# Performance work log

Measured on AMD Instinct MI355X. Metric: run time of the kernel, lower is better.

## Reference

```python
import jax, jax.numpy as jnp
import numpy as np

E, D, H, K = 8, 768, 3072, 2   # num_experts, embed_size, expert_size, top-k
TAU = 1.0
BN, PN = 32, 196

def l2norm(v):
    # F.normalize(p=2, dim=-1), eps=1e-12
    return v / jnp.maximum(jnp.linalg.norm(v, axis=-1, keepdims=True), 1e-12)

def setup_inputs() -> dict:
    key = jax.random.key(0)
    ks = jax.random.split(key, 8)
    s = 0.02  # weight init scale for stability
    return {
        "x": jax.random.normal(ks[0], (BN, PN, D), dtype=jnp.float32),
        "Wlinear": jax.random.normal(ks[1], (D, D), dtype=jnp.float32) * s,
        "learnedE": jax.random.normal(ks[2], (E, D), dtype=jnp.float32),
        "bias": jnp.zeros((BN * PN, E), dtype=jnp.float32),
        "W1": jax.random.normal(ks[3], (E, D, H), dtype=jnp.float32) * s,
        "b1": jnp.zeros((E, H), dtype=jnp.float32),
        "W2": jax.random.normal(ks[4], (E, H, D), dtype=jnp.float32) * s,
        "b2": jnp.zeros((E, D), dtype=jnp.float32),
        "sW1": jax.random.normal(ks[5], (D, H), dtype=jnp.float32) * s,
        "sb1": jnp.zeros((H,), dtype=jnp.float32),
        "sW2": jax.random.normal(ks[6], (H, D), dtype=jnp.float32) * s,
        "sb2": jnp.zeros((D,), dtype=jnp.float32),
    }

def reference(x, Wlinear, learnedE, bias, W1, b1, W2, b2, sW1, sb1, sW2, sb2):
    bn, pn, d = x.shape
    patches = x.reshape(bn * pn, d)                      # [T, D]
    proj = l2norm(patches @ Wlinear.T)                   # router projection
    routed = proj @ l2norm(learnedE).T                   # [T, E] cosine scores
    probs = jax.nn.softmax((routed + bias) / TAU, axis=1)  # eval path (no noise)
    k_probs, k_idx = jax.lax.top_k(probs, K)             # [T, K]
    # combine weights: scatter top-k probs into dense [T, E] gate matrix
    T = probs.shape[0]
    gates = jnp.zeros_like(probs).at[jnp.arange(T)[:, None], k_idx].add(k_probs)
    # expert MLPs computed densely for all experts, masked by gates
    h = jax.nn.gelu(jnp.einsum('td,edh->teh', patches, W1) + b1[None], approximate=False)
    eo = jnp.einsum('teh,ehd->ted', h, W2) + b2[None]    # [T, E, D]
    moe = jnp.einsum('ted,te->td', eo, gates)            # weighted combine
    # shared expert (expert_list[-1]) applied to every token; dropout is identity in eval
    shared = jax.nn.gelu(patches @ sW1 + sb1, approximate=False) @ sW2 + sb2
    return (moe + shared).reshape(bn, pn, d)
```

## Files before the change

### kernel.cpp

```cpp
#include <hip/hip_runtime.h>
#include <hip/hip_bf16.h>

typedef __hip_bfloat16 bf16;
typedef __attribute__((ext_vector_type(8))) short short8;
typedef __attribute__((ext_vector_type(4))) float f32x4;

#define T_TOK 6272
#define D_DIM 768
#define H_DIM 3072
#define NEXP 8
#define MAXTILES 160
#define BKR 64

#define S_BARRIER() __builtin_amdgcn_s_barrier()
#define WAIT_VM4() asm volatile("s_waitcnt vmcnt(4)" ::: "memory")
#define WAIT_VM0() asm volatile("s_waitcnt vmcnt(0)" ::: "memory")
#define WAIT_LGKM0() asm volatile("s_waitcnt lgkmcnt(0)" ::: "memory")

__device__ __forceinline__ void async16(void* lds, const void* g) {
  __builtin_amdgcn_global_load_lds(
      (const __attribute__((address_space(1))) void*)g,
      (__attribute__((address_space(3))) void*)lds, 16, 0, 0);
}

__device__ __forceinline__ float gelu_f(float x) {
  float z = x * 0.70710678118654752f;
  float az = fabsf(z);
  float t = 1.f / (1.f + 0.3275911f * az);
  float poly = ((((1.061405429f * t - 1.453152027f) * t + 1.421413741f) * t -
                 0.284496736f) * t + 0.254829592f) * t;
  float e = __expf(-az * az);
  float er = 1.f - poly * e;
  er = copysignf(er, z);
  return 0.5f * x * (1.f + er);
}


__global__ void cast_hilo(const float* __restrict__ in, bf16* __restrict__ hi,
                          bf16* __restrict__ lo, int n) {
  int i = blockIdx.x * blockDim.x + threadIdx.x;
  int stride = gridDim.x * blockDim.x;
  for (; i < n; i += stride) {
    float x = in[i];
    bf16 h = __float2bfloat16(x);
    hi[i] = h;
    lo[i] = __float2bfloat16(x - __bfloat162float(h));
  }
}

__global__ void transpose_cast(const float* __restrict__ in, bf16* __restrict__ out,
                               int R, int C) {
  __shared__ float tile[32][33];
  int b = blockIdx.z;
  const float* ib = in + (size_t)b * R * C;
  bf16* ob = out + (size_t)b * R * C;
  int r0 = blockIdx.x * 32, c0 = blockIdx.y * 32;
  int tx = threadIdx.x & 31, ty = threadIdx.x >> 5;
  for (int i = 0; i < 32; i += 8)
    tile[ty + i][tx] = ib[(size_t)(r0 + ty + i) * C + c0 + tx];
  __syncthreads();
  for (int i = 0; i < 32; i += 8)
    ob[(size_t)(c0 + ty + i) * R + r0 + tx] = __float2bfloat16(tile[tx][ty + i]);
}

__global__ void norm_learnedE(const float* __restrict__ lE, float* __restrict__ eHat) {
  int wave = threadIdx.x >> 6, lane = threadIdx.x & 63;
  for (int e = wave; e < NEXP; e += 4) {
    float v[12];
    float ss = 0.f;
    for (int j = 0; j < 12; j++) {
      v[j] = lE[e * D_DIM + lane + 64 * j];
      ss += v[j] * v[j];
    }
    for (int o = 32; o; o >>= 1) ss += __shfl_xor(ss, o);
    float rn = 1.f / fmaxf(sqrtf(ss), 1e-12f);
    for (int j = 0; j < 12; j++) eHat[e * D_DIM + lane + 64 * j] = v[j] * rn;
  }
}


__global__ __launch_bounds__(256, 2) void gemm_router(
    const bf16* __restrict__ pHi, const bf16* __restrict__ pLo,
    const bf16* __restrict__ wHi, const bf16* __restrict__ wLo,
    float* __restrict__ y) {
  __shared__ __align__(16) bf16 As[2][128 * BKR];
  __shared__ __align__(16) bf16 Bs[2][128 * BKR];
  int tid = threadIdx.x, wave = tid >> 6, lane = tid & 63;
  int wr = wave >> 1, wc = wave & 1;
  int rowbase = blockIdx.x * 128, colbase = blockIdx.y * 128;
  int rslot = (lane & 7) ^ (lane >> 3);

  size_t aoff[4], boff[4];
#pragma unroll
  for (int c = 0; c < 4; c++) {
    int row = 32 * wave + 8 * c + (lane >> 3);
    aoff[c] = (size_t)(rowbase + row) * D_DIM + rslot * 8;
    boff[c] = (size_t)(colbase + row) * D_DIM + rslot * 8;
  }

  auto stage = [&](int buf, int ks) {
    int term = ks / 12;
    const bf16* A = (term == 1) ? pLo : pHi;
    const bf16* B = (term == 2) ? wLo : wHi;
    int kk = (ks - term * 12) * BKR;
#pragma unroll
    for (int c = 0; c < 4; c++) {
      async16(&As[buf][(32 * wave + 8 * c) * BKR], A + aoff[c] + kk);
      async16(&Bs[buf][(32 * wave + 8 * c) * BKR], B + boff[c] + kk);
    }
  };

  f32x4 acc[4][4];
#pragma unroll
  for (int m = 0; m < 4; m++)
#pragma unroll
    for (int n = 0; n < 4; n++) acc[m][n] = 0.f;

  stage(0, 0);
  __syncthreads();
  int cur = 0;
  int q = lane >> 4, fr = lane & 15;
  for (int ks = 0; ks < 36; ks++) {
    if (ks < 35) stage(cur ^ 1, ks + 1);
    const bf16* Ac = As[cur];
    const bf16* Bc = Bs[cur];
#pragma unroll
    for (int kh = 0; kh < 2; kh++) {
      short8 af[4], bfr[4];
#pragma unroll
      for (int m = 0; m < 4; m++) {
        int row = wr * 64 + m * 16 + fr;
        int ls = ((kh << 2) + q) ^ (row & 7);
        af[m] = *(const short8*)&Ac[row * BKR + ls * 8];
      }
#pragma unroll
      for (int n = 0; n < 4; n++) {
        int row = wc * 64 + n * 16 + fr;
        int ls = ((kh << 2) + q) ^ (row & 7);
        bfr[n] = *(const short8*)&Bc[row * BKR + ls * 8];
      }
#pragma unroll
      for (int m = 0; m < 4; m++)
#pragma unroll
        for (int n = 0; n < 4; n++)
          acc[m][n] = __builtin_amdgcn_mfma_f32_16x16x32_bf16(af[m], bfr[n], acc[m][n], 0, 0, 0);
    }
    __syncthreads();
    cur ^= 1;
  }
  for (int m = 0; m < 4; m++)
    for (int n = 0; n < 4; n++)
      for (int j = 0; j < 4; j++) {
        int r = rowbase + wr * 64 + m * 16 + (lane >> 4) * 4 + j;
        int c = colbase + wc * 64 + n * 16 + (lane & 15);
        y[(size_t)r * D_DIM + c] = acc[m][n][j];
      }
}


__global__ void router_epi(const float* __restrict__ y, const float* __restrict__ eHat,
                           const float* __restrict__ bias, int* __restrict__ gidx,
                           float* __restrict__ gval, int* __restrict__ counts) {
  int wave = threadIdx.x >> 6, lane = threadIdx.x & 63;
  int t = blockIdx.x * 4 + wave;
  float v[12];
  float ss = 0.f;
  for (int j = 0; j < 12; j++) {
    v[j] = y[(size_t)t * D_DIM + lane + 64 * j];
    ss += v[j] * v[j];
  }
  for (int o = 32; o; o >>= 1) ss += __shfl_xor(ss, o);
  float d[NEXP];
  for (int e = 0; e < NEXP; e++) {
    float s = 0.f;
    for (int j = 0; j < 12; j++) s += v[j] * eHat[e * D_DIM + lane + 64 * j];
    for (int o = 32; o; o >>= 1) s += __shfl_xor(s, o);
    d[e] = s;
  }
  if (lane == 0) {
    float rn = 1.f / fmaxf(sqrtf(ss), 1e-12f);
    float sc[NEXP], mx = -1e30f;
    for (int e = 0; e < NEXP; e++) {
      sc[e] = d[e] * rn + bias[t * NEXP + e];
      mx = fmaxf(mx, sc[e]);
    }
    float p[NEXP], sum = 0.f;
    for (int e = 0; e < NEXP; e++) {
      p[e] = expf(sc[e] - mx);
      sum += p[e];
    }
    float inv = 1.f / sum;
    int i1 = 0;
    for (int e = 1; e < NEXP; e++)
      if (sc[e] > sc[i1]) i1 = e;
    int i2 = -1;
    for (int e = 0; e < NEXP; e++) {
      if (e == i1) continue;
      if (i2 < 0 || sc[e] > sc[i2]) i2 = e;
    }
    gidx[t * 2] = i1;
    gidx[t * 2 + 1] = i2;
    gval[t * 2] = p[i1] * inv;
    gval[t * 2 + 1] = p[i2] * inv;
    atomicAdd(&counts[i1], 1);
    atomicAdd(&counts[i2], 1);
  }
}


__global__ void scan_build(const int* __restrict__ counts, int* __restrict__ segstart,
                           int* __restrict__ cursors, int* __restrict__ tiles,
                           int* __restrict__ numtiles) {
  if (threadIdx.x == 0) {
    int off = 0;
    for (int e = 0; e < NEXP; e++) {
      segstart[e] = off;
      cursors[e] = off;
      off += counts[e];
    }
    segstart[NEXP] = off;
    segstart[NEXP + 1] = off + T_TOK;
    int nt = 0;
    for (int e = 0; e < NEXP + 1; e++) {
      int cnt = (e < NEXP) ? counts[e] : T_TOK;
      int ntl = (cnt + 127) >> 7;
      for (int l = 0; l < ntl; l++) {
        tiles[nt * 2] = e;
        tiles[nt * 2 + 1] = l;
        nt++;
      }
    }
    *numtiles = nt;
  }
}

__global__ void fill_assign(const int* __restrict__ gidx, int* __restrict__ cursors,
                            int* __restrict__ rowtok, int* __restrict__ slot_of) {
  int t = blockIdx.x * 256 + threadIdx.x;
  if (t >= T_TOK) return;
  for (int k = 0; k < 2; k++) {
    int e = gidx[t * 2 + k];
    int pos = atomicAdd(&cursors[e], 1);
    rowtok[pos] = t;
    slot_of[t * 2 + k] = pos;
  }
  rowtok[2 * T_TOK + t] = t;
}



__global__ __launch_bounds__(256, 4) void gemm_ffn1(
    const bf16* __restrict__ pHi, const bf16* __restrict__ W1T,
    const bf16* __restrict__ sW1T, const float* __restrict__ b1,
    const float* __restrict__ sb1, const int* __restrict__ segstart,
    const int* __restrict__ tiles, const int* __restrict__ numtiles,
    const int* __restrict__ rowtok, bf16* __restrict__ hbuf) {
  int gx = blockIdx.x;
  if (gx >= *numtiles) return;
  int seg = tiles[gx * 2], lt = tiles[gx * 2 + 1];
  int s0 = segstart[seg] + lt * 128;
  int send = segstart[seg + 1];
  const bf16* Bw = (seg < NEXP) ? W1T + (size_t)seg * H_DIM * D_DIM : sW1T;
  const float* bb = (seg < NEXP) ? b1 + seg * H_DIM : sb1;

  __shared__ __align__(16) bf16 As[2][128 * 32];
  __shared__ __align__(16) bf16 Bs[2][128 * 32];
  int tid = threadIdx.x, wave = tid >> 6, lane = tid & 63;
  int wr = wave >> 1, wc = wave & 1;
  int colbase = blockIdx.y * 128;
  int g8 = (((lane & 3) ^ ((lane >> 3) & 3))) * 8;

  const bf16* aptr[2];
  const bf16* bptr[2];
#pragma unroll
  for (int p = 0; p < 2; p++) {
    int r = wave * 32 + p * 16 + (lane >> 2);
    int s = s0 + r;
    if (s > send - 1) s = send - 1;
    aptr[p] = pHi + (size_t)rowtok[s] * D_DIM + g8;
    bptr[p] = Bw + (size_t)(colbase + r) * D_DIM + g8;
  }

  auto stage = [&](int buf, int ks) {
    int kk = ks * 32;
#pragma unroll
    for (int p = 0; p < 2; p++) {
      async16(&As[buf][(wave * 32 + p * 16) * 32], aptr[p] + kk);
      async16(&Bs[buf][(wave * 32 + p * 16) * 32], bptr[p] + kk);
    }
  };

  f32x4 acc[4][4];
#pragma unroll
  for (int m = 0; m < 4; m++)
#pragma unroll
    for (int n = 0; n < 4; n++) acc[m][n] = 0.f;

  WAIT_VM0();
  stage(0, 0);
  stage(1, 1);

  int q = lane >> 4, fr = lane & 15;
  int ls8 = (q ^ ((fr >> 1) & 3)) * 8;

#define NT1 24
  for (int ks = 0; ks < NT1; ks++) {
    if (ks + 1 < NT1) { WAIT_VM4(); } else { WAIT_VM0(); }
    S_BARRIER();
    const bf16* Ac = As[ks & 1];
    const bf16* Bc = Bs[ks & 1];
    short8 af[4], bfr[4];
#pragma unroll
    for (int m = 0; m < 4; m++)
      af[m] = *(const short8*)&Ac[(wr * 64 + m * 16 + fr) * 32 + ls8];
#pragma unroll
    for (int n = 0; n < 4; n++)
      bfr[n] = *(const short8*)&Bc[(wc * 64 + n * 16 + fr) * 32 + ls8];
    __builtin_amdgcn_s_setprio(1);
#pragma unroll
    for (int m = 0; m < 4; m++)
#pragma unroll
      for (int n = 0; n < 4; n++)
        acc[m][n] = __builtin_amdgcn_mfma_f32_16x16x32_bf16(af[m], bfr[n], acc[m][n], 0, 0, 0);
    __builtin_amdgcn_s_setprio(0);
    WAIT_LGKM0();
    S_BARRIER();
    if (ks + 2 < NT1) stage(ks & 1, ks + 2);
  }
#pragma unroll
  for (int n = 0; n < 4; n++) {
    int c = colbase + wc * 64 + n * 16 + (lane & 15);
    float bv = bb[c];
#pragma unroll
    for (int m = 0; m < 4; m++)
#pragma unroll
      for (int j = 0; j < 4; j++) {
        int s = s0 + wr * 64 + m * 16 + (lane >> 4) * 4 + j;
        if (s < send) {
          float xv = acc[m][n][j] + bv;
          hbuf[(size_t)s * H_DIM + c] = __float2bfloat16(gelu_f(xv));
        }
      }
  }
}


__global__ __launch_bounds__(256, 4) void gemm_ffn2(
    const bf16* __restrict__ hbuf, const bf16* __restrict__ W2T,
    const bf16* __restrict__ sW2T, const float* __restrict__ b2,
    const float* __restrict__ sb2, const int* __restrict__ segstart,
    const int* __restrict__ tiles, const int* __restrict__ numtiles,
    float* __restrict__ moebuf) {
  int gx = blockIdx.x;
  if (gx >= *numtiles) return;
  int seg = tiles[gx * 2], lt = tiles[gx * 2 + 1];
  int s0 = segstart[seg] + lt * 128;
  int send = segstart[seg + 1];
  const bf16* Bw = (seg < NEXP) ? W2T + (size_t)seg * H_DIM * D_DIM : sW2T;
  const float* bb = (seg < NEXP) ? b2 + seg * D_DIM : sb2;

  __shared__ __align__(16) bf16 As[2][128 * 32];
  __shared__ __align__(16) bf16 Bs[2][128 * 32];
  int tid = threadIdx.x, wave = tid >> 6, lane = tid & 63;
  int wr = wave >> 1, wc = wave & 1;
  int colbase = blockIdx.y * 128;
  int g8 = (((lane & 3) ^ ((lane >> 3) & 3))) * 8;

  const bf16* aptr[2];
  const bf16* bptr[2];
#pragma unroll
  for (int p = 0; p < 2; p++) {
    int r = wave * 32 + p * 16 + (lane >> 2);
    int s = s0 + r;
    if (s > send - 1) s = send - 1;
    aptr[p] = hbuf + (size_t)s * H_DIM + g8;
    bptr[p] = Bw + (size_t)(colbase + r) * H_DIM + g8;
  }

  auto stage = [&](int buf, int ks) {
    int kk = ks * 32;
#pragma unroll
    for (int p = 0; p < 2; p++) {
      async16(&As[buf][(wave * 32 + p * 16) * 32], aptr[p] + kk);
      async16(&Bs[buf][(wave * 32 + p * 16) * 32], bptr[p] + kk);
    }
  };

  f32x4 acc[4][4];
#pragma unroll
  for (int m = 0; m < 4; m++)
#pragma unroll
    for (int n = 0; n < 4; n++) acc[m][n] = 0.f;

  WAIT_VM0();
  stage(0, 0);
  stage(1, 1);

  int q = lane >> 4, fr = lane & 15;
  int ls8 = (q ^ ((fr >> 1) & 3)) * 8;

#define NT2 96
  for (int ks = 0; ks < NT2; ks++) {
    if (ks + 1 < NT2) { WAIT_VM4(); } else { WAIT_VM0(); }
    S_BARRIER();
    const bf16* Ac = As[ks & 1];
    const bf16* Bc = Bs[ks & 1];
    short8 af[4], bfr[4];
#pragma unroll
    for (int m = 0; m < 4; m++)
      af[m] = *(const short8*)&Ac[(wr * 64 + m * 16 + fr) * 32 + ls8];
#pragma unroll
    for (int n = 0; n < 4; n++)
      bfr[n] = *(const short8*)&Bc[(wc * 64 + n * 16 + fr) * 32 + ls8];
    __builtin_amdgcn_s_setprio(1);
#pragma unroll
    for (int m = 0; m < 4; m++)
#pragma unroll
      for (int n = 0; n < 4; n++)
        acc[m][n] = __builtin_amdgcn_mfma_f32_16x16x32_bf16(af[m], bfr[n], acc[m][n], 0, 0, 0);
    __builtin_amdgcn_s_setprio(0);
    WAIT_LGKM0();
    S_BARRIER();
    if (ks + 2 < NT2) stage(ks & 1, ks + 2);
  }
#pragma unroll
  for (int n = 0; n < 4; n++) {
    int c = colbase + wc * 64 + n * 16 + (lane & 15);
    float bv = bb[c];
#pragma unroll
    for (int m = 0; m < 4; m++)
#pragma unroll
      for (int j = 0; j < 4; j++) {
        int s = s0 + wr * 64 + m * 16 + (lane >> 4) * 4 + j;
        if (s < send) moebuf[(size_t)s * D_DIM + c] = acc[m][n][j] + bv;
      }
  }
}


__global__ void combine_out(const float* __restrict__ moebuf, const float* __restrict__ gval,
                            const int* __restrict__ slot_of, float* __restrict__ out) {
  int i = blockIdx.x * 256 + threadIdx.x;
  const int total = T_TOK * (D_DIM / 4);
  if (i >= total) return;
  int t = i / (D_DIM / 4), c = i % (D_DIM / 4);
  float g0 = gval[2 * t], g1 = gval[2 * t + 1];
  int sA = slot_of[2 * t], sB = slot_of[2 * t + 1];
  const f32x4* pa = (const f32x4*)(moebuf + (size_t)sA * D_DIM) + c;
  const f32x4* pb = (const f32x4*)(moebuf + (size_t)sB * D_DIM) + c;
  const f32x4* ps = (const f32x4*)(moebuf + (size_t)(2 * T_TOK + t) * D_DIM) + c;
  f32x4 r = g0 * (*pa) + g1 * (*pb) + *ps;
  ((f32x4*)out)[i] = r;
}


extern "C" void kernel_launch(void* const* d_in, const int* in_sizes, int n_in,
                              void* d_out, int out_size, void* d_ws, size_t ws_size,
                              hipStream_t stream) {
  const float* x = (const float*)d_in[0];
  const float* Wlinear = (const float*)d_in[1];
  const float* learnedE = (const float*)d_in[2];
  const float* bias = (const float*)d_in[3];
  const float* W1 = (const float*)d_in[4];
  const float* b1 = (const float*)d_in[5];
  const float* W2 = (const float*)d_in[6];
  const float* b2 = (const float*)d_in[7];
  const float* sW1 = (const float*)d_in[8];
  const float* sb1 = (const float*)d_in[9];
  const float* sW2 = (const float*)d_in[10];
  const float* sb2 = (const float*)d_in[11];
  float* out = (float*)d_out;

  char* ws = (char*)d_ws;
  size_t off = 0;
  auto alloc = [&](size_t bytes) {
    char* p = ws + off;
    off += (bytes + 255) & ~(size_t)255;
    return p;
  };
  float* eHat = (float*)alloc(8 * 768 * 4);
  bf16* pHi = (bf16*)alloc((size_t)T_TOK * D_DIM * 2);
  bf16* pLo = (bf16*)alloc((size_t)T_TOK * D_DIM * 2);
  bf16* wHi = (bf16*)alloc((size_t)D_DIM * D_DIM * 2);
  bf16* wLo = (bf16*)alloc((size_t)D_DIM * D_DIM * 2);
  bf16* W1T = (bf16*)alloc((size_t)NEXP * D_DIM * H_DIM * 2);
  bf16* W2T = (bf16*)alloc((size_t)NEXP * D_DIM * H_DIM * 2);
  bf16* sW1T = (bf16*)alloc((size_t)D_DIM * H_DIM * 2);
  bf16* sW2T = (bf16*)alloc((size_t)D_DIM * H_DIM * 2);
  float* y = (float*)alloc((size_t)T_TOK * D_DIM * 4);
  bf16* hbuf = (bf16*)alloc((size_t)3 * T_TOK * H_DIM * 2);
  float* moebuf = (float*)alloc((size_t)3 * T_TOK * D_DIM * 4);
  int* gidx = (int*)alloc(T_TOK * 2 * 4);
  float* gval = (float*)alloc(T_TOK * 2 * 4);
  int* rowtok = (int*)alloc(3 * T_TOK * 4);
  int* slot_of = (int*)alloc(T_TOK * 2 * 4);
  int* counts = (int*)alloc(8 * 4);
  int* segstart = (int*)alloc(10 * 4);
  int* cursors = (int*)alloc(8 * 4);
  int* numtiles = (int*)alloc(4);
  int* tiles = (int*)alloc(MAXTILES * 2 * 4);
  (void)ws_size; (void)in_sizes; (void)n_in; (void)out_size;

  hipMemsetAsync(counts, 0, 8 * 4, stream);
  norm_learnedE<<<1, 256, 0, stream>>>(learnedE, eHat);
  cast_hilo<<<2048, 256, 0, stream>>>(x, pHi, pLo, T_TOK * D_DIM);
  cast_hilo<<<1024, 256, 0, stream>>>(Wlinear, wHi, wLo, D_DIM * D_DIM);
  transpose_cast<<<dim3(D_DIM / 32, H_DIM / 32, NEXP), 256, 0, stream>>>(W1, W1T, D_DIM, H_DIM);
  transpose_cast<<<dim3(H_DIM / 32, D_DIM / 32, NEXP), 256, 0, stream>>>(W2, W2T, H_DIM, D_DIM);
  transpose_cast<<<dim3(D_DIM / 32, H_DIM / 32, 1), 256, 0, stream>>>(sW1, sW1T, D_DIM, H_DIM);
  transpose_cast<<<dim3(H_DIM / 32, D_DIM / 32, 1), 256, 0, stream>>>(sW2, sW2T, H_DIM, D_DIM);

  gemm_router<<<dim3(T_TOK / 128, D_DIM / 128), 256, 0, stream>>>(pHi, pLo, wHi, wLo, y);
  router_epi<<<T_TOK / 4, 256, 0, stream>>>(y, eHat, bias, gidx, gval, counts);
  scan_build<<<1, 64, 0, stream>>>(counts, segstart, cursors, tiles, numtiles);
  fill_assign<<<(T_TOK + 255) / 256, 256, 0, stream>>>(gidx, cursors, rowtok, slot_of);

  gemm_ffn1<<<dim3(MAXTILES, H_DIM / 128), 256, 0, stream>>>(
      pHi, W1T, sW1T, b1, sb1, segstart, tiles, numtiles, rowtok, hbuf);
  gemm_ffn2<<<dim3(MAXTILES, D_DIM / 128), 256, 0, stream>>>(
      hbuf, W2T, sW2T, b2, sb2, segstart, tiles, numtiles, moebuf);

  combine_out<<<(T_TOK * (D_DIM / 4) + 255) / 256, 256, 0, stream>>>(moebuf, gval, slot_of, out);
}
```

Baseline: 723.1 us.

## Enlarge expert FFN GEMM tiles to 256x256x64 with 512-thread blocks

```diff
diff --git a/kernel.cpp b/kernel.cpp
--- a/kernel.cpp
+++ b/kernel.cpp
@@ -9,11 +9,11 @@
 #define D_DIM 768
 #define H_DIM 3072
 #define NEXP 8
-#define MAXTILES 160
+#define MAXT 96
 #define BKR 64
 
 #define S_BARRIER() __builtin_amdgcn_s_barrier()
-#define WAIT_VM4() asm volatile("s_waitcnt vmcnt(4)" ::: "memory")
+#define WAIT_VM8() asm volatile("s_waitcnt vmcnt(8)" ::: "memory")
 #define WAIT_VM0() asm volatile("s_waitcnt vmcnt(0)" ::: "memory")
 #define WAIT_LGKM0() asm volatile("s_waitcnt lgkmcnt(0)" ::: "memory")
 
@@ -223,7 +223,7 @@
     int nt = 0;
     for (int e = 0; e < NEXP + 1; e++) {
       int cnt = (e < NEXP) ? counts[e] : T_TOK;
-      int ntl = (cnt + 127) >> 7;
+      int ntl = (cnt + 255) >> 8;
       for (int l = 0; l < ntl; l++) {
         tiles[nt * 2] = e;
         tiles[nt * 2 + 1] = l;
@@ -249,7 +249,7 @@
 
 
 
-__global__ __launch_bounds__(256, 4) void gemm_ffn1(
+__global__ __launch_bounds__(512, 2) void gemm_ffn1(
     const bf16* __restrict__ pHi, const bf16* __restrict__ W1T,
     const bf16* __restrict__ sW1T, const float* __restrict__ b1,
     const float* __restrict__ sb1, const int* __restrict__ segstart,
@@ -258,41 +258,41 @@
   int gx = blockIdx.x;
   if (gx >= *numtiles) return;
   int seg = tiles[gx * 2], lt = tiles[gx * 2 + 1];
-  int s0 = segstart[seg] + lt * 128;
+  int s0 = segstart[seg] + lt * 256;
   int send = segstart[seg + 1];
   const bf16* Bw = (seg < NEXP) ? W1T + (size_t)seg * H_DIM * D_DIM : sW1T;
   const float* bb = (seg < NEXP) ? b1 + seg * H_DIM : sb1;
 
-  __shared__ __align__(16) bf16 As[2][128 * 32];
-  __shared__ __align__(16) bf16 Bs[2][128 * 32];
+  __shared__ __align__(16) bf16 As[2][256 * 64];
+  __shared__ __align__(16) bf16 Bs[2][256 * 64];
   int tid = threadIdx.x, wave = tid >> 6, lane = tid & 63;
-  int wr = wave >> 1, wc = wave & 1;
-  int colbase = blockIdx.y * 128;
-  int g8 = (((lane & 3) ^ ((lane >> 3) & 3))) * 8;
-
-  const bf16* aptr[2];
-  const bf16* bptr[2];
-#pragma unroll
-  for (int p = 0; p < 2; p++) {
-    int r = wave * 32 + p * 16 + (lane >> 2);
+  int wr = wave >> 2, wc = wave & 3;
+  int colbase = blockIdx.y * 256;
+  int g8 = ((lane & 7) ^ (lane >> 3)) * 8;
+
+  const bf16* aptr[4];
+  const bf16* bptr[4];
+#pragma unroll
+  for (int j = 0; j < 4; j++) {
+    int r = wave * 32 + j * 8 + (lane >> 3);
     int s = s0 + r;
     if (s > send - 1) s = send - 1;
-    aptr[p] = pHi + (size_t)rowtok[s] * D_DIM + g8;
-    bptr[p] = Bw + (size_t)(colbase + r) * D_DIM + g8;
-  }
-
-  auto stage = [&](int buf, int ks) {
-    int kk = ks * 32;
-#pragma unroll
-    for (int p = 0; p < 2; p++) {
-      async16(&As[buf][(wave * 32 + p * 16) * 32], aptr[p] + kk);
-      async16(&Bs[buf][(wave * 32 + p * 16) * 32], bptr[p] + kk);
+    aptr[j] = pHi + (size_t)rowtok[s] * D_DIM + g8;
+    bptr[j] = Bw + (size_t)(colbase + r) * D_DIM + g8;
+  }
+
+  auto stage = [&](int buf, int kt) {
+    int kk = kt * 64;
+#pragma unroll
+    for (int j = 0; j < 4; j++) {
+      async16(&As[buf][(wave * 32 + j * 8) * 64], aptr[j] + kk);
+      async16(&Bs[buf][(wave * 32 + j * 8) * 64], bptr[j] + kk);
     }
   };
 
-  f32x4 acc[4][4];
-#pragma unroll
-  for (int m = 0; m < 4; m++)
+  f32x4 acc[8][4];
+#pragma unroll
+  for (int m = 0; m < 8; m++)
 #pragma unroll
     for (int n = 0; n < 4; n++) acc[m][n] = 0.f;
 
@@ -301,41 +301,44 @@
   stage(1, 1);
 
   int q = lane >> 4, fr = lane & 15;
-  int ls8 = (q ^ ((fr >> 1) & 3)) * 8;
-
-#define NT1 24
-  for (int ks = 0; ks < NT1; ks++) {
-    if (ks + 1 < NT1) { WAIT_VM4(); } else { WAIT_VM0(); }
+  int frs = fr & 7;
+
+#define NT1 12
+  for (int kt = 0; kt < NT1; kt++) {
+    if (kt + 1 < NT1) { WAIT_VM8(); } else { WAIT_VM0(); }
     S_BARRIER();
-    const bf16* Ac = As[ks & 1];
-    const bf16* Bc = Bs[ks & 1];
-    short8 af[4], bfr[4];
-#pragma unroll
-    for (int m = 0; m < 4; m++)
-      af[m] = *(const short8*)&Ac[(wr * 64 + m * 16 + fr) * 32 + ls8];
-#pragma unroll
-    for (int n = 0; n < 4; n++)
-      bfr[n] = *(const short8*)&Bc[(wc * 64 + n * 16 + fr) * 32 + ls8];
-    __builtin_amdgcn_s_setprio(1);
-#pragma unroll
-    for (int m = 0; m < 4; m++)
-#pragma unroll
-      for (int n = 0; n < 4; n++)
-        acc[m][n] = __builtin_amdgcn_mfma_f32_16x16x32_bf16(af[m], bfr[n], acc[m][n], 0, 0, 0);
-    __builtin_amdgcn_s_setprio(0);
+    const bf16* Ac = As[kt & 1];
+    const bf16* Bc = Bs[kt & 1];
+#pragma unroll
+    for (int kh = 0; kh < 2; kh++) {
+      int ls8 = (((kh << 2) + q) ^ frs) * 8;
+      short8 af[8];
+#pragma unroll
+      for (int m = 0; m < 8; m++)
+        af[m] = *(const short8*)&Ac[(wr * 128 + m * 16 + fr) * 64 + ls8];
+      __builtin_amdgcn_s_setprio(1);
+#pragma unroll
+      for (int n = 0; n < 4; n++) {
+        short8 bfr = *(const short8*)&Bc[(wc * 64 + n * 16 + fr) * 64 + ls8];
+#pragma unroll
+        for (int m = 0; m < 8; m++)
+          acc[m][n] = __builtin_amdgcn_mfma_f32_16x16x32_bf16(af[m], bfr, acc[m][n], 0, 0, 0);
+      }
+      __builtin_amdgcn_s_setprio(0);
+    }
     WAIT_LGKM0();
     S_BARRIER();
-    if (ks + 2 < NT1) stage(ks & 1, ks + 2);
+    if (kt + 2 < NT1) stage(kt & 1, kt + 2);
   }
 #pragma unroll
   for (int n = 0; n < 4; n++) {
-    int c = colbase + wc * 64 + n * 16 + (lane & 15);
+    int c = colbase + wc * 64 + n * 16 + fr;
     float bv = bb[c];
 #pragma unroll
-    for (int m = 0; m < 4; m++)
+    for (int m = 0; m < 8; m++)
 #pragma unroll
       for (int j = 0; j < 4; j++) {
-        int s = s0 + wr * 64 + m * 16 + (lane >> 4) * 4 + j;
+        int s = s0 + wr * 128 + m * 16 + q * 4 + j;
         if (s < send) {
           float xv = acc[m][n][j] + bv;
           hbuf[(size_t)s * H_DIM + c] = __float2bfloat16(gelu_f(xv));
@@ -345,7 +348,7 @@
 }
 
 
-__global__ __launch_bounds__(256, 4) void gemm_ffn2(
+__global__ __launch_bounds__(512, 2) void gemm_ffn2(
     const bf16* __restrict__ hbuf, const bf16* __restrict__ W2T,
     const bf16* __restrict__ sW2T, const float* __restrict__ b2,
     const float* __restrict__ sb2, const int* __restrict__ segstart,
@@ -354,41 +357,41 @@
   int gx = blockIdx.x;
   if (gx >= *numtiles) return;
   int seg = tiles[gx * 2], lt = tiles[gx * 2 + 1];
-  int s0 = segstart[seg] + lt * 128;
+  int s0 = segstart[seg] + lt * 256;
   int send = segstart[seg + 1];
   const bf16* Bw = (seg < NEXP) ? W2T + (size_t)seg * H_DIM * D_DIM : sW2T;
   const float* bb = (seg < NEXP) ? b2 + seg * D_DIM : sb2;
 
-  __shared__ __align__(16) bf16 As[2][128 * 32];
-  __shared__ __align__(16) bf16 Bs[2][128 * 32];
+  __shared__ __align__(16) bf16 As[2][256 * 64];
+  __shared__ __align__(16) bf16 Bs[2][256 * 64];
   int tid = threadIdx.x, wave = tid >> 6, lane = tid & 63;
-  int wr = wave >> 1, wc = wave & 1;
-  int colbase = blockIdx.y * 128;
-  int g8 = (((lane & 3) ^ ((lane >> 3) & 3))) * 8;
-
-  const bf16* aptr[2];
-  const bf16* bptr[2];
-#pragma unroll
-  for (int p = 0; p < 2; p++) {
-    int r = wave * 32 + p * 16 + (lane >> 2);
+  int wr = wave >> 2, wc = wave & 3;
+  int colbase = blockIdx.y * 256;
+  int g8 = ((lane & 7) ^ (lane >> 3)) * 8;
+
+  const bf16* aptr[4];
+  const bf16* bptr[4];
+#pragma unroll
+  for (int j = 0; j < 4; j++) {
+    int r = wave * 32 + j * 8 + (lane >> 3);
     int s = s0 + r;
     if (s > send - 1) s = send - 1;
-    aptr[p] = hbuf + (size_t)s * H_DIM + g8;
-    bptr[p] = Bw + (size_t)(colbase + r) * H_DIM + g8;
-  }
-
-  auto stage = [&](int buf, int ks) {
-    int kk = ks * 32;
-#pragma unroll
-    for (int p = 0; p < 2; p++) {
-      async16(&As[buf][(wave * 32 + p * 16) * 32], aptr[p] + kk);
-      async16(&Bs[buf][(wave * 32 + p * 16) * 32], bptr[p] + kk);
+    aptr[j] = hbuf + (size_t)s * H_DIM + g8;
+    bptr[j] = Bw + (size_t)(colbase + r) * H_DIM + g8;
+  }
+
+  auto stage = [&](int buf, int kt) {
+    int kk = kt * 64;
+#pragma unroll
+    for (int j = 0; j < 4; j++) {
+      async16(&As[buf][(wave * 32 + j * 8) * 64], aptr[j] + kk);
+      async16(&Bs[buf][(wave * 32 + j * 8) * 64], bptr[j] + kk);
     }
   };
 
-  f32x4 acc[4][4];
-#pragma unroll
-  for (int m = 0; m < 4; m++)
+  f32x4 acc[8][4];
+#pragma unroll
+  for (int m = 0; m < 8; m++)
 #pragma unroll
     for (int n = 0; n < 4; n++) acc[m][n] = 0.f;
 
@@ -397,41 +400,44 @@
   stage(1, 1);
 
   int q = lane >> 4, fr = lane & 15;
-  int ls8 = (q ^ ((fr >> 1) & 3)) * 8;
-
-#define NT2 96
-  for (int ks = 0; ks < NT2; ks++) {
-    if (ks + 1 < NT2) { WAIT_VM4(); } else { WAIT_VM0(); }
+  int frs = fr & 7;
+
+#define NT2 48
+  for (int kt = 0; kt < NT2; kt++) {
+    if (kt + 1 < NT2) { WAIT_VM8(); } else { WAIT_VM0(); }
     S_BARRIER();
-    const bf16* Ac = As[ks & 1];
-    const bf16* Bc = Bs[ks & 1];
-    short8 af[4], bfr[4];
-#pragma unroll
-    for (int m = 0; m < 4; m++)
-      af[m] = *(const short8*)&Ac[(wr * 64 + m * 16 + fr) * 32 + ls8];
-#pragma unroll
-    for (int n = 0; n < 4; n++)
-      bfr[n] = *(const short8*)&Bc[(wc * 64 + n * 16 + fr) * 32 + ls8];
-    __builtin_amdgcn_s_setprio(1);
-#pragma unroll
-    for (int m = 0; m < 4; m++)
-#pragma unroll
-      for (int n = 0; n < 4; n++)
-        acc[m][n] = __builtin_amdgcn_mfma_f32_16x16x32_bf16(af[m], bfr[n], acc[m][n], 0, 0, 0);
-    __builtin_amdgcn_s_setprio(0);
+    const bf16* Ac = As[kt & 1];
+    const bf16* Bc = Bs[kt & 1];
+#pragma unroll
+    for (int kh = 0; kh < 2; kh++) {
+      int ls8 = (((kh << 2) + q) ^ frs) * 8;
+      short8 af[8];
+#pragma unroll
+      for (int m = 0; m < 8; m++)
+        af[m] = *(const short8*)&Ac[(wr * 128 + m * 16 + fr) * 64 + ls8];
+      __builtin_amdgcn_s_setprio(1);
+#pragma unroll
+      for (int n = 0; n < 4; n++) {
+        short8 bfr = *(const short8*)&Bc[(wc * 64 + n * 16 + fr) * 64 + ls8];
+#pragma unroll
+        for (int m = 0; m < 8; m++)
+          acc[m][n] = __builtin_amdgcn_mfma_f32_16x16x32_bf16(af[m], bfr, acc[m][n], 0, 0, 0);
+      }
+      __builtin_amdgcn_s_setprio(0);
+    }
     WAIT_LGKM0();
     S_BARRIER();
-    if (ks + 2 < NT2) stage(ks & 1, ks + 2);
+    if (kt + 2 < NT2) stage(kt & 1, kt + 2);
   }
 #pragma unroll
   for (int n = 0; n < 4; n++) {
-    int c = colbase + wc * 64 + n * 16 + (lane & 15);
+    int c = colbase + wc * 64 + n * 16 + fr;
     float bv = bb[c];
 #pragma unroll
-    for (int m = 0; m < 4; m++)
+    for (int m = 0; m < 8; m++)
 #pragma unroll
       for (int j = 0; j < 4; j++) {
-        int s = s0 + wr * 64 + m * 16 + (lane >> 4) * 4 + j;
+        int s = s0 + wr * 128 + m * 16 + q * 4 + j;
         if (s < send) moebuf[(size_t)s * D_DIM + c] = acc[m][n][j] + bv;
       }
   }
@@ -498,7 +504,7 @@
   int* segstart = (int*)alloc(10 * 4);
   int* cursors = (int*)alloc(8 * 4);
   int* numtiles = (int*)alloc(4);
-  int* tiles = (int*)alloc(MAXTILES * 2 * 4);
+  int* tiles = (int*)alloc(MAXT * 2 * 4);
   (void)ws_size; (void)in_sizes; (void)n_in; (void)out_size;
 
   hipMemsetAsync(counts, 0, 8 * 4, stream);
@@ -515,9 +521,9 @@
   scan_build<<<1, 64, 0, stream>>>(counts, segstart, cursors, tiles, numtiles);
   fill_assign<<<(T_TOK + 255) / 256, 256, 0, stream>>>(gidx, cursors, rowtok, slot_of);
 
-  gemm_ffn1<<<dim3(MAXTILES, H_DIM / 128), 256, 0, stream>>>(
+  gemm_ffn1<<<dim3(MAXT, H_DIM / 256), 512, 0, stream>>>(
       pHi, W1T, sW1T, b1, sb1, segstart, tiles, numtiles, rowtok, hbuf);
-  gemm_ffn2<<<dim3(MAXTILES, D_DIM / 128), 256, 0, stream>>>(
+  gemm_ffn2<<<dim3(MAXT, D_DIM / 256), 512, 0, stream>>>(
       hbuf, W2T, sW2T, b2, sb2, segstart, tiles, numtiles, moebuf);
 
   combine_out<<<(T_TOK * (D_DIM / 4) + 255) / 256, 256, 0, stream>>>(moebuf, gval, slot_of, out);
```

After: 825.2 us. +14.1%, slower.

## Load A fragments directly from global to registers, stage only B in LDS

Applied to the files above, without the earlier changes.

```diff
diff --git a/kernel.cpp b/kernel.cpp
--- a/kernel.cpp
+++ b/kernel.cpp
@@ -13,7 +13,7 @@
 #define BKR 64
 
 #define S_BARRIER() __builtin_amdgcn_s_barrier()
-#define WAIT_VM4() asm volatile("s_waitcnt vmcnt(4)" ::: "memory")
+#define WAIT_VM2() asm volatile("s_waitcnt vmcnt(2)" ::: "memory")
 #define WAIT_VM0() asm volatile("s_waitcnt vmcnt(0)" ::: "memory")
 #define WAIT_LGKM0() asm volatile("s_waitcnt lgkmcnt(0)" ::: "memory")
 
@@ -263,31 +263,33 @@
   const bf16* Bw = (seg < NEXP) ? W1T + (size_t)seg * H_DIM * D_DIM : sW1T;
   const float* bb = (seg < NEXP) ? b1 + seg * H_DIM : sb1;
 
-  __shared__ __align__(16) bf16 As[2][128 * 32];
   __shared__ __align__(16) bf16 Bs[2][128 * 32];
   int tid = threadIdx.x, wave = tid >> 6, lane = tid & 63;
   int wr = wave >> 1, wc = wave & 1;
   int colbase = blockIdx.y * 128;
+  int q = lane >> 4, fr = lane & 15;
   int g8 = (((lane & 3) ^ ((lane >> 3) & 3))) * 8;
-
-  const bf16* aptr[2];
+  int ls8 = (q ^ ((fr >> 1) & 3)) * 8;
+
   const bf16* bptr[2];
 #pragma unroll
   for (int p = 0; p < 2; p++) {
     int r = wave * 32 + p * 16 + (lane >> 2);
-    int s = s0 + r;
+    bptr[p] = Bw + (size_t)(colbase + r) * D_DIM + g8;
+  }
+  const bf16* arow[4];
+#pragma unroll
+  for (int m = 0; m < 4; m++) {
+    int s = s0 + wr * 64 + m * 16 + fr;
     if (s > send - 1) s = send - 1;
-    aptr[p] = pHi + (size_t)rowtok[s] * D_DIM + g8;
-    bptr[p] = Bw + (size_t)(colbase + r) * D_DIM + g8;
-  }
-
-  auto stage = [&](int buf, int ks) {
+    arow[m] = pHi + (size_t)rowtok[s] * D_DIM + q * 8;
+  }
+
+  auto stageB = [&](int buf, int ks) {
     int kk = ks * 32;
 #pragma unroll
-    for (int p = 0; p < 2; p++) {
-      async16(&As[buf][(wave * 32 + p * 16) * 32], aptr[p] + kk);
+    for (int p = 0; p < 2; p++)
       async16(&Bs[buf][(wave * 32 + p * 16) * 32], bptr[p] + kk);
-    }
   };
 
   f32x4 acc[4][4];
@@ -297,22 +299,18 @@
     for (int n = 0; n < 4; n++) acc[m][n] = 0.f;
 
   WAIT_VM0();
-  stage(0, 0);
-  stage(1, 1);
-
-  int q = lane >> 4, fr = lane & 15;
-  int ls8 = (q ^ ((fr >> 1) & 3)) * 8;
+  short8 af[4];
+#pragma unroll
+  for (int m = 0; m < 4; m++) af[m] = *(const short8*)arow[m];
+  stageB(0, 0);
+  stageB(1, 1);
 
 #define NT1 24
   for (int ks = 0; ks < NT1; ks++) {
-    if (ks + 1 < NT1) { WAIT_VM4(); } else { WAIT_VM0(); }
+    if (ks + 1 < NT1) { WAIT_VM2(); } else { WAIT_VM0(); }
     S_BARRIER();
-    const bf16* Ac = As[ks & 1];
     const bf16* Bc = Bs[ks & 1];
-    short8 af[4], bfr[4];
-#pragma unroll
-    for (int m = 0; m < 4; m++)
-      af[m] = *(const short8*)&Ac[(wr * 64 + m * 16 + fr) * 32 + ls8];
+    short8 bfr[4];
 #pragma unroll
     for (int n = 0; n < 4; n++)
       bfr[n] = *(const short8*)&Bc[(wc * 64 + n * 16 + fr) * 32 + ls8];
@@ -325,17 +323,22 @@
     __builtin_amdgcn_s_setprio(0);
     WAIT_LGKM0();
     S_BARRIER();
-    if (ks + 2 < NT1) stage(ks & 1, ks + 2);
+    if (ks + 1 < NT1) {
+      int kk = (ks + 1) * 32;
+#pragma unroll
+      for (int m = 0; m < 4; m++) af[m] = *(const short8*)(arow[m] + kk);
+      if (ks + 2 < NT1) stageB(ks & 1, ks + 2);
+    }
   }
 #pragma unroll
   for (int n = 0; n < 4; n++) {
-    int c = colbase + wc * 64 + n * 16 + (lane & 15);
+    int c = colbase + wc * 64 + n * 16 + fr;
     float bv = bb[c];
 #pragma unroll
     for (int m = 0; m < 4; m++)
 #pragma unroll
       for (int j = 0; j < 4; j++) {
-        int s = s0 + wr * 64 + m * 16 + (lane >> 4) * 4 + j;
+        int s = s0 + wr * 64 + m * 16 + q * 4 + j;
         if (s < send) {
           float xv = acc[m][n][j] + bv;
           hbuf[(size_t)s * H_DIM + c] = __float2bfloat16(gelu_f(xv));
@@ -359,31 +362,33 @@
   const bf16* Bw = (seg < NEXP) ? W2T + (size_t)seg * H_DIM * D_DIM : sW2T;
   const float* bb = (seg < NEXP) ? b2 + seg * D_DIM : sb2;
 
-  __shared__ __align__(16) bf16 As[2][128 * 32];
   __shared__ __align__(16) bf16 Bs[2][128 * 32];
   int tid = threadIdx.x, wave = tid >> 6, lane = tid & 63;
   int wr = wave >> 1, wc = wave & 1;
   int colbase = blockIdx.y * 128;
+  int q = lane >> 4, fr = lane & 15;
   int g8 = (((lane & 3) ^ ((lane >> 3) & 3))) * 8;
-
-  const bf16* aptr[2];
+  int ls8 = (q ^ ((fr >> 1) & 3)) * 8;
+
   const bf16* bptr[2];
 #pragma unroll
   for (int p = 0; p < 2; p++) {
     int r = wave * 32 + p * 16 + (lane >> 2);
-    int s = s0 + r;
+    bptr[p] = Bw + (size_t)(colbase + r) * H_DIM + g8;
+  }
+  const bf16* arow[4];
+#pragma unroll
+  for (int m = 0; m < 4; m++) {
+    int s = s0 + wr * 64 + m * 16 + fr;
     if (s > send - 1) s = send - 1;
-    aptr[p] = hbuf + (size_t)s * H_DIM + g8;
-    bptr[p] = Bw + (size_t)(colbase + r) * H_DIM + g8;
-  }
-
-  auto stage = [&](int buf, int ks) {
+    arow[m] = hbuf + (size_t)s * H_DIM + q * 8;
+  }
+
+  auto stageB = [&](int buf, int ks) {
     int kk = ks * 32;
 #pragma unroll
-    for (int p = 0; p < 2; p++) {
-      async16(&As[buf][(wave * 32 + p * 16) * 32], aptr[p] + kk);
+    for (int p = 0; p < 2; p++)
       async16(&Bs[buf][(wave * 32 + p * 16) * 32], bptr[p] + kk);
-    }
   };
 
   f32x4 acc[4][4];
@@ -393,22 +398,18 @@
     for (int n = 0; n < 4; n++) acc[m][n] = 0.f;
 
   WAIT_VM0();
-  stage(0, 0);
-  stage(1, 1);
-
-  int q = lane >> 4, fr = lane & 15;
-  int ls8 = (q ^ ((fr >> 1) & 3)) * 8;
+  short8 af[4];
+#pragma unroll
+  for (int m = 0; m < 4; m++) af[m] = *(const short8*)arow[m];
+  stageB(0, 0);
+  stageB(1, 1);
 
 #define NT2 96
   for (int ks = 0; ks < NT2; ks++) {
-    if (ks + 1 < NT2) { WAIT_VM4(); } else { WAIT_VM0(); }
+    if (ks + 1 < NT2) { WAIT_VM2(); } else { WAIT_VM0(); }
     S_BARRIER();
-    const bf16* Ac = As[ks & 1];
     const bf16* Bc = Bs[ks & 1];
-    short8 af[4], bfr[4];
-#pragma unroll
-    for (int m = 0; m < 4; m++)
-      af[m] = *(const short8*)&Ac[(wr * 64 + m * 16 + fr) * 32 + ls8];
+    short8 bfr[4];
 #pragma unroll
     for (int n = 0; n < 4; n++)
       bfr[n] = *(const short8*)&Bc[(wc * 64 + n * 16 + fr) * 32 + ls8];
@@ -421,17 +422,22 @@
     __builtin_amdgcn_s_setprio(0);
     WAIT_LGKM0();
     S_BARRIER();
-    if (ks + 2 < NT2) stage(ks & 1, ks + 2);
+    if (ks + 1 < NT2) {
+      int kk = (ks + 1) * 32;
+#pragma unroll
+      for (int m = 0; m < 4; m++) af[m] = *(const short8*)(arow[m] + kk);
+      if (ks + 2 < NT2) stageB(ks & 1, ks + 2);
+    }
   }
 #pragma unroll
   for (int n = 0; n < 4; n++) {
-    int c = colbase + wc * 64 + n * 16 + (lane & 15);
+    int c = colbase + wc * 64 + n * 16 + fr;
     float bv = bb[c];
 #pragma unroll
     for (int m = 0; m < 4; m++)
 #pragma unroll
       for (int j = 0; j < 4; j++) {
-        int s = s0 + wr * 64 + m * 16 + (lane >> 4) * 4 + j;
+        int s = s0 + wr * 64 + m * 16 + q * 4 + j;
         if (s < send) moebuf[(size_t)s * D_DIM + c] = acc[m][n][j] + bv;
       }
   }
```

Result: slower. 860.8 us (+19.1%).

## Widen FFN1 GEMM tile to 128x256 with triple-buffered async LDS staging

Applied to the files above, without the earlier changes.

```diff
diff --git a/kernel.cpp b/kernel.cpp
--- a/kernel.cpp
+++ b/kernel.cpp
@@ -13,6 +13,8 @@
 #define BKR 64
 
 #define S_BARRIER() __builtin_amdgcn_s_barrier()
+#define WAIT_VM12() asm volatile("s_waitcnt vmcnt(12)" ::: "memory")
+#define WAIT_VM6() asm volatile("s_waitcnt vmcnt(6)" ::: "memory")
 #define WAIT_VM4() asm volatile("s_waitcnt vmcnt(4)" ::: "memory")
 #define WAIT_VM0() asm volatile("s_waitcnt vmcnt(0)" ::: "memory")
 #define WAIT_LGKM0() asm volatile("s_waitcnt lgkmcnt(0)" ::: "memory")
@@ -248,8 +250,7 @@
 }
 
 
-
-__global__ __launch_bounds__(256, 4) void gemm_ffn1(
+__global__ __launch_bounds__(256, 2) void gemm_ffn1(
     const bf16* __restrict__ pHi, const bf16* __restrict__ W1T,
     const bf16* __restrict__ sW1T, const float* __restrict__ b1,
     const float* __restrict__ sb1, const int* __restrict__ segstart,
@@ -263,79 +264,85 @@
   const bf16* Bw = (seg < NEXP) ? W1T + (size_t)seg * H_DIM * D_DIM : sW1T;
   const float* bb = (seg < NEXP) ? b1 + seg * H_DIM : sb1;
 
-  __shared__ __align__(16) bf16 As[2][128 * 32];
-  __shared__ __align__(16) bf16 Bs[2][128 * 32];
+  __shared__ __align__(16) bf16 As[3][128 * 32];
+  __shared__ __align__(16) bf16 Bs[3][256 * 32];
   int tid = threadIdx.x, wave = tid >> 6, lane = tid & 63;
   int wr = wave >> 1, wc = wave & 1;
-  int colbase = blockIdx.y * 128;
+  int colbase = blockIdx.y * 256;
+  int q = lane >> 4, fr = lane & 15;
   int g8 = (((lane & 3) ^ ((lane >> 3) & 3))) * 8;
+  int ls8 = (q ^ ((fr >> 1) & 3)) * 8;
 
   const bf16* aptr[2];
-  const bf16* bptr[2];
 #pragma unroll
   for (int p = 0; p < 2; p++) {
     int r = wave * 32 + p * 16 + (lane >> 2);
     int s = s0 + r;
     if (s > send - 1) s = send - 1;
     aptr[p] = pHi + (size_t)rowtok[s] * D_DIM + g8;
-    bptr[p] = Bw + (size_t)(colbase + r) * D_DIM + g8;
+  }
+  const bf16* bptr[4];
+#pragma unroll
+  for (int j = 0; j < 4; j++) {
+    int r = wave * 64 + j * 16 + (lane >> 2);
+    bptr[j] = Bw + (size_t)(colbase + r) * D_DIM + g8;
   }
 
   auto stage = [&](int buf, int ks) {
     int kk = ks * 32;
 #pragma unroll
-    for (int p = 0; p < 2; p++) {
+    for (int p = 0; p < 2; p++)
       async16(&As[buf][(wave * 32 + p * 16) * 32], aptr[p] + kk);
-      async16(&Bs[buf][(wave * 32 + p * 16) * 32], bptr[p] + kk);
-    }
+#pragma unroll
+    for (int j = 0; j < 4; j++)
+      async16(&Bs[buf][(wave * 64 + j * 16) * 32], bptr[j] + kk);
   };
 
-  f32x4 acc[4][4];
+  f32x4 acc[4][8];
 #pragma unroll
   for (int m = 0; m < 4; m++)
 #pragma unroll
-    for (int n = 0; n < 4; n++) acc[m][n] = 0.f;
+    for (int n = 0; n < 8; n++) acc[m][n] = 0.f;
 
   WAIT_VM0();
   stage(0, 0);
   stage(1, 1);
-
-  int q = lane >> 4, fr = lane & 15;
-  int ls8 = (q ^ ((fr >> 1) & 3)) * 8;
+  stage(2, 2);
 
 #define NT1 24
   for (int ks = 0; ks < NT1; ks++) {
-    if (ks + 1 < NT1) { WAIT_VM4(); } else { WAIT_VM0(); }
+    if (ks + 2 < NT1) { WAIT_VM12(); }
+    else if (ks + 1 < NT1) { WAIT_VM6(); }
+    else { WAIT_VM0(); }
     S_BARRIER();
-    const bf16* Ac = As[ks & 1];
-    const bf16* Bc = Bs[ks & 1];
-    short8 af[4], bfr[4];
+    const bf16* Ac = As[ks % 3];
+    const bf16* Bc = Bs[ks % 3];
+    short8 af[4];
 #pragma unroll
     for (int m = 0; m < 4; m++)
       af[m] = *(const short8*)&Ac[(wr * 64 + m * 16 + fr) * 32 + ls8];
-#pragma unroll
-    for (int n = 0; n < 4; n++)
-      bfr[n] = *(const short8*)&Bc[(wc * 64 + n * 16 + fr) * 32 + ls8];
     __builtin_amdgcn_s_setprio(1);
 #pragma unroll
-    for (int m = 0; m < 4; m++)
-#pragma unroll
-      for (int n = 0; n < 4; n++)
-        acc[m][n] = __builtin_amdgcn_mfma_f32_16x16x32_bf16(af[m], bfr[n], acc[m][n], 0, 0, 0);
+    for (int n = 0; n < 8; n++) {
+      short8 bfr = *(const short8*)&Bc[(wc * 128 + n * 16 + fr) * 32 + ls8];
+#pragma unroll
+      for (int m = 0; m < 4; m++)
+        acc[m][n] = __builtin_amdgcn_mfma_f32_16x16x32_bf16(af[m], bfr, acc[m][n], 0, 0, 0);
+    }
     __builtin_amdgcn_s_setprio(0);
     WAIT_LGKM0();
     S_BARRIER();
-    if (ks + 2 < NT1) stage(ks & 1, ks + 2);
-  }
-#pragma unroll
-  for (int n = 0; n < 4; n++) {
-    int c = colbase + wc * 64 + n * 16 + (lane & 15);
+    if (ks + 3 < NT1) stage(ks % 3, ks + 3);
+  }
+#pragma unroll
+  for (int n = 0; n < 8; n++) {
+    int c = colbase + wc * 128 + n * 16 + fr;
     float bv = bb[c];
 #pragma unroll
     for (int m = 0; m < 4; m++)
 #pragma unroll
       for (int j = 0; j < 4; j++) {
-        int s = s0 + wr * 64 + m * 16 + (lane >> 4) * 4 + j;
+        int s = s0 + wr * 64 + m * 16 + q * 4 + j;
         if (s < send) {
           float xv = acc[m][n][j] + bv;
           hbuf[(size_t)s * H_DIM + c] = __float2bfloat16(gelu_f(xv));
@@ -515,7 +522,7 @@
   scan_build<<<1, 64, 0, stream>>>(counts, segstart, cursors, tiles, numtiles);
   fill_assign<<<(T_TOK + 255) / 256, 256, 0, stream>>>(gidx, cursors, rowtok, slot_of);
 
-  gemm_ffn1<<<dim3(MAXTILES, H_DIM / 128), 256, 0, stream>>>(
+  gemm_ffn1<<<dim3(MAXTILES, H_DIM / 256), 256, 0, stream>>>(
       pHi, W1T, sW1T, b1, sb1, segstart, tiles, numtiles, rowtok, hbuf);
   gemm_ffn2<<<dim3(MAXTILES, D_DIM / 128), 256, 0, stream>>>(
       hbuf, W2T, sW2T, b2, sb2, segstart, tiles, numtiles, moebuf);
```

Result: slower. 740.3 us (+2.4%).
